# Kernel tuning notes

Measured on AMD Instinct MI355X. Metric: run time of the kernel, lower is better.

Reference implementation:

```python
import jax, jax.numpy as jnp
import numpy as np

B, C, H, W = 1, 64, 128, 128
HEADS, NWIN, TOPK = 8, 16, 4
EPS = 1e-6


def dwconv(x, w, b, pad):
    # x: NCHW, w: (C,1,k,k) depthwise conv weight
    y = jax.lax.conv_general_dilated(
        x, w, (1, 1), [(pad, pad), (pad, pad)],
        dimension_numbers=('NCHW', 'OIHW', 'NCHW'),
        feature_group_count=x.shape[1])
    return y + b[None, :, None, None]


def layernorm(x, g, b):
    m = x.mean(-1, keepdims=True)
    v = ((x - m) ** 2).mean(-1, keepdims=True)
    return (x - m) * jax.lax.rsqrt(v + EPS) * g + b


def drf_attn(x, qkv_w, qkv_b, wo_w, wo_b, lepe_w, lepe_b):
    # x: (B,H,W,C) NHWC, BiFormer-style top-k routed window attention
    Bb, Hh, Ww, Cc = x.shape
    h, w = Hh // NWIN, Ww // NWIN
    hw, p2 = h * w, NWIN * NWIN
    # window partition -> (B, p2, hw, C)
    xw = x.reshape(Bb, NWIN, h, NWIN, w, Cc).transpose(0, 1, 3, 2, 4, 5).reshape(Bb, p2, hw, Cc)
    qkv = xw @ qkv_w + qkv_b                       # (B,p2,hw,3C), qk_dim == dim
    q, kv = qkv[..., :Cc], qkv[..., Cc:]
    # window-level routing: per-window mean q/k
    q_win = q.mean(2)                              # (B,p2,C)
    k_win = kv[..., :Cc].mean(2)                   # (B,p2,C)
    logits = jnp.einsum('bpc,bqc->bpq', q_win, k_win)
    _, idx = jax.lax.top_k(logits, TOPK)           # (B,p2,TOPK) int32
    # gather top-k kv windows for each query window -> (B,p2,TOPK,hw,2C)
    kv_sel = jax.vmap(lambda kvb, ib: kvb[ib])(kv, idx)
    hd = Cc // HEADS
    k_sel = kv_sel[..., :Cc].reshape(Bb, p2, TOPK * hw, HEADS, hd).transpose(0, 1, 3, 2, 4)
    v_sel = kv_sel[..., Cc:].reshape(Bb, p2, TOPK * hw, HEADS, hd).transpose(0, 1, 3, 2, 4)
    q_h = q.reshape(Bb, p2, hw, HEADS, hd).transpose(0, 1, 3, 2, 4)
    scale = Cc ** -0.5                             # qk_dim ** -0.5 as in torch module
    attn = jax.nn.softmax(jnp.einsum('bpnqd,bpnkd->bpnqk', q_h * scale, k_sel), axis=-1)
    out = jnp.einsum('bpnqk,bpnkd->bpnqd', attn, v_sel)
    out = out.transpose(0, 1, 3, 2, 4).reshape(Bb, p2, hw, Cc)
    # un-window -> (B,H,W,C)
    out = out.reshape(Bb, NWIN, NWIN, h, w, Cc).transpose(0, 1, 3, 2, 4, 5).reshape(Bb, Hh, Ww, Cc)
    # LePE: depthwise 5x5 conv on full-image v
    v_full = kv[..., Cc:].reshape(Bb, NWIN, NWIN, h, w, Cc).transpose(0, 1, 3, 2, 4, 5).reshape(Bb, Hh, Ww, Cc)
    lepe = dwconv(v_full.transpose(0, 3, 1, 2), lepe_w, lepe_b, 2).transpose(0, 2, 3, 1)
    return (out + lepe) @ wo_w + wo_b


def setup_inputs() -> dict:
    key = jax.random.key(0)
    ks = jax.random.split(key, 8)
    s = lambda k, shape: jax.random.normal(k, shape, jnp.float32) * 0.02
    return {
        'x': jax.random.normal(ks[0], (B, C, H, W), jnp.float32),
        'pos_w': s(ks[1], (C, 1, 3, 3)), 'pos_b': jnp.zeros((C,), jnp.float32),
        'norm_g': jnp.ones((C,), jnp.float32), 'norm_b': jnp.zeros((C,), jnp.float32),
        'qkv_w': s(ks[2], (C, 3 * C)), 'qkv_b': jnp.zeros((3 * C,), jnp.float32),
        'wo_w': s(ks[3], (C, C)), 'wo_b': jnp.zeros((C,), jnp.float32),
        'lepe_w': s(ks[4], (C, 1, 5, 5)), 'lepe_b': jnp.zeros((C,), jnp.float32),
        'mlp_w1': s(ks[5], (C, 4 * C)), 'mlp_b1': jnp.zeros((4 * C,), jnp.float32),
        'mlp_w2': s(ks[6], (4 * C, C)), 'mlp_b2': jnp.zeros((C,), jnp.float32),
    }


def reference(x, pos_w, pos_b, norm_g, norm_b, qkv_w, qkv_b, wo_w, wo_b,
              lepe_w, lepe_b, mlp_w1, mlp_b1, mlp_w2, mlp_b2):
    x = x + dwconv(x, pos_w, pos_b, 1)             # dwconv pos-embed (NCHW)
    x = x.transpose(0, 2, 3, 1)                    # -> NHWC
    x = x + drf_attn(layernorm(x, norm_g, norm_b), qkv_w, qkv_b, wo_w, wo_b, lepe_w, lepe_b)
    y = layernorm(x, norm_g, norm_b)               # same LayerNorm weights reused
    y = jax.nn.gelu(y @ mlp_w1 + mlp_b1, approximate=False) @ mlp_w2 + mlp_b2
    x = x + y
    return x.transpose(0, 3, 1, 2)                 # -> NCHW
```

## Files before the change

kernel.cpp:

```cpp
#include <hip/hip_runtime.h>
#include <hip/hip_bf16.h>
#include <math.h>

#define HPIX 128
#define WPIX 128
#define NPIX (HPIX*WPIX)
#define CCH 64
#define P2 256
#define HWIN 64
#define LNS 36
#define LNS2 68

__device__ __forceinline__ float waveReduceSum(float v){
  #pragma unroll
  for (int m = 32; m >= 1; m >>= 1) v += __shfl_xor(v, m);
  return v;
}

__device__ __forceinline__ float gelu_exact(float h){
  return 0.5f*h*(1.f + erff(h*0.70710678118654752f));
}

__global__ void k1_posconv(const float* __restrict__ x, const float* __restrict__ pw,
                           const float* __restrict__ pb, float* __restrict__ x1){
  __shared__ float tile[4][3][72];
  __shared__ float lds[4][64];
  int tid = threadIdx.x;
  int pl = tid & 63, cl = tid >> 6;
  int pix0 = (blockIdx.x & 255) * 64;
  int cg   = (blockIdx.x >> 8);
  int c = cg*4 + cl;
  int y  = pix0 >> 7;
  int xb = pix0 & 127;
  const float* xc = x + c*NPIX;
  for (int t = pl; t < 3*66; t += 64){
    int r = t / 66, ccol = t - r*66;
    int yy = y - 1 + r, xxr = xb - 1 + ccol;
    float v = 0.f;
    if ((unsigned)yy < (unsigned)HPIX && (unsigned)xxr < (unsigned)WPIX)
      v = xc[yy*WPIX + xxr];
    tile[cl][r][ccol] = v;
  }
  float wreg[9];
  #pragma unroll
  for (int t=0;t<9;t++) wreg[t] = pw[c*9+t];
  float bias = pb[c];
  __syncthreads();
  float acc = bias;
  #pragma unroll
  for (int dy=0;dy<3;dy++)
    #pragma unroll
    for (int dx=0;dx<3;dx++)
      acc += wreg[dy*3+dx] * tile[cl][dy][pl+dx];
  lds[cl][pl] = tile[cl][1][pl+1] + acc;
  __syncthreads();
  int pp = tid >> 2, cc = tid & 3;
  x1[(pix0+pp)*CCH + cg*4 + cc] = lds[cc][pp];
}

__global__ void k2_ln_qkv(const float* __restrict__ x1,
                          const float* __restrict__ g, const float* __restrict__ bb,
                          const float* __restrict__ qw, const float* __restrict__ qb,
                          float* __restrict__ qkv){
  __shared__ __align__(16) float lnT[64][LNS2];
  int tid = threadIdx.x, w = tid >> 6, lane = tid & 63;
  int pix0 = blockIdx.x * 64;
  #pragma unroll
  for (int i=0; i<8; i++){
    int pl = w*8 + i, pix = pix0 + pl;
    float v = x1[pix*CCH + lane];
    float mean = waveReduceSum(v) * (1.f/64.f);
    float d = v - mean;
    float var = waveReduceSum(d*d) * (1.f/64.f);
    lnT[lane][pl] = d * rsqrtf(var + 1e-6f) * g[lane] + bb[lane];
  }
  __syncthreads();
  int p0 = (tid & 15) * 4;
  int cg = tid >> 4;
  int j0 = cg * 6;
  float acc[4][6];
  #pragma unroll
  for (int i=0;i<4;i++)
    #pragma unroll
    for (int j=0;j<6;j++) acc[i][j] = qb[j0+j];
  for (int k0=0; k0<64; k0+=2){
    float4 a0 = *(const float4*)&lnT[k0][p0];
    float4 a1 = *(const float4*)&lnT[k0+1][p0];
    const float* wr0 = qw + k0*192 + j0;
    const float* wr1 = wr0 + 192;
    float2 u00 = *(const float2*)(wr0);
    float2 u01 = *(const float2*)(wr0+2);
    float2 u02 = *(const float2*)(wr0+4);
    float2 u10 = *(const float2*)(wr1);
    float2 u11 = *(const float2*)(wr1+2);
    float2 u12 = *(const float2*)(wr1+4);
    float a0v[4] = {a0.x,a0.y,a0.z,a0.w};
    float a1v[4] = {a1.x,a1.y,a1.z,a1.w};
    #pragma unroll
    for (int i=0;i<4;i++){
      acc[i][0]+=a0v[i]*u00.x; acc[i][1]+=a0v[i]*u00.y;
      acc[i][2]+=a0v[i]*u01.x; acc[i][3]+=a0v[i]*u01.y;
      acc[i][4]+=a0v[i]*u02.x; acc[i][5]+=a0v[i]*u02.y;
    }
    #pragma unroll
    for (int i=0;i<4;i++){
      acc[i][0]+=a1v[i]*u10.x; acc[i][1]+=a1v[i]*u10.y;
      acc[i][2]+=a1v[i]*u11.x; acc[i][3]+=a1v[i]*u11.y;
      acc[i][4]+=a1v[i]*u12.x; acc[i][5]+=a1v[i]*u12.y;
    }
  }
  int y = pix0 >> 7;
  int pb_row = (y>>3)*16, rrow = (y&7)<<3, xbase = pix0 & 127;
  #pragma unroll
  for (int i=0;i<4;i++){
    int xx = xbase + p0 + i;
    int p = pb_row + (xx>>3);
    int r = rrow + (xx&7);
    float* o = qkv + (p*HWIN + r)*192 + j0;
    *(float2*)(o)     = make_float2(acc[i][0], acc[i][1]);
    *(float2*)(o + 2) = make_float2(acc[i][2], acc[i][3]);
    *(float2*)(o + 4) = make_float2(acc[i][4], acc[i][5]);
  }
}

__global__ void k3_winmean(const float* __restrict__ qkv,
                           float* __restrict__ qwin, float* __restrict__ kwinT){
  int p = blockIdx.x;
  int tid = threadIdx.x, rq = tid >> 6, c = tid & 63;
  float sq = 0.f, sk = 0.f;
  for (int r = rq*16; r < rq*16+16; r++){
    const float* row = qkv + (p*HWIN + r)*192;
    sq += row[c];
    sk += row[64 + c];
  }
  __shared__ float s1[4][64], s2[4][64];
  s1[rq][c] = sq; s2[rq][c] = sk;
  __syncthreads();
  if (tid < 64){
    qwin[p*64 + c]   = (s1[0][c]+s1[1][c]+s1[2][c]+s1[3][c])*(1.f/64.f);
    kwinT[c*P2 + p]  = (s2[0][c]+s2[1][c]+s2[2][c]+s2[3][c])*(1.f/64.f);
  }
}

__global__ void k4_topk(const float* __restrict__ qwin, const float* __restrict__ kwinT,
                        int* __restrict__ idx){
  int p = blockIdx.x, t = threadIdx.x;
  int w = t >> 6, lane = t & 63;
  __shared__ float qs[64];
  __shared__ float lg[P2];
  __shared__ float wv[4]; __shared__ int wi[4];
  if (t < 64) qs[t] = qwin[p*64 + t];
  __syncthreads();
  float acc = 0.f;
  #pragma unroll 8
  for (int c=0; c<64; c++) acc += qs[c] * kwinT[c*P2 + t];
  lg[t] = acc;
  __syncthreads();
  for (int j=0; j<4; j++){
    float v = lg[t]; int i = t;
    #pragma unroll
    for (int m=32; m>=1; m>>=1){
      float ov = __shfl_xor(v, m); int oi = __shfl_xor(i, m);
      if (ov > v || (ov == v && oi < i)){ v = ov; i = oi; }
    }
    if (lane == 0){ wv[w] = v; wi[w] = i; }
    __syncthreads();
    if (t == 0){
      float bv = wv[0]; int bi = wi[0];
      #pragma unroll
      for (int u=1; u<4; u++)
        if (wv[u] > bv || (wv[u] == bv && wi[u] < bi)){ bv = wv[u]; bi = wi[u]; }
      idx[p*4 + j] = bi;
      lg[bi] = -1e30f;
    }
    __syncthreads();
  }
}

__global__ void k5_attn(const float* __restrict__ qkv, const int* __restrict__ idx,
                        float* __restrict__ attnout){
  int p = blockIdx.x >> 3, n = blockIdx.x & 7;
  int tid = threadIdx.x, w = tid >> 6, lane = tid & 63;
  __shared__ float Ks[256][8];
  __shared__ float Vs[256][8];
  __shared__ int wsel[4];
  float* psbuf = &Ks[0][0];
  __shared__ float ps_tail[256];
  (void)ps_tail;
  if (tid < 4) wsel[tid] = idx[p*4 + tid];
  __syncthreads();
  int cb = n*8;
  for (int u = tid; u < 512; u += 256){
    int k = u >> 1, h = u & 1;
    const float* row = qkv + (wsel[k>>6]*HWIN + (k&63))*192;
    *(float4*)&Ks[k][h*4] = *(const float4*)(row + 64  + cb + h*4);
    *(float4*)&Vs[k][h*4] = *(const float4*)(row + 128 + cb + h*4);
  }
  __syncthreads();
  const float* qrow = qkv + (p*HWIN + lane)*192 + cb;
  float4 q0 = *(const float4*)(qrow);
  float4 q1 = *(const float4*)(qrow + 4);
  float q[8] = {q0.x*0.125f, q0.y*0.125f, q0.z*0.125f, q0.w*0.125f,
                q1.x*0.125f, q1.y*0.125f, q1.z*0.125f, q1.w*0.125f};
  float l = 0.f, acc[8];
  #pragma unroll
  for (int d=0; d<8; d++) acc[d] = 0.f;
  #pragma unroll 4
  for (int k = w*64; k < w*64+64; k++){
    float4 ka = *(float4*)&Ks[k][0];
    float4 kb = *(float4*)&Ks[k][4];
    float s = q[0]*ka.x + q[1]*ka.y + q[2]*ka.z + q[3]*ka.w
            + q[4]*kb.x + q[5]*kb.y + q[6]*kb.z + q[7]*kb.w;
    float e = __expf(s);
    l += e;
    float4 va = *(float4*)&Vs[k][0];
    float4 vb = *(float4*)&Vs[k][4];
    acc[0]+=e*va.x; acc[1]+=e*va.y; acc[2]+=e*va.z; acc[3]+=e*va.w;
    acc[4]+=e*vb.x; acc[5]+=e*vb.y; acc[6]+=e*vb.z; acc[7]+=e*vb.w;
  }
  __syncthreads();
  float* myp = psbuf + (w*64 + lane)*9;
  #pragma unroll
  for (int d=0; d<8; d++) myp[d] = acc[d];
  myp[8] = l;
  __syncthreads();
  {
    int qi = (w << 4) + (lane & 15);
    int d0 = (lane >> 4) * 2;
    float L = 0.f, o0 = 0.f, o1 = 0.f;
    #pragma unroll
    for (int u=0; u<4; u++){
      const float* pp2 = psbuf + (u*64 + qi)*9;
      L  += pp2[8];
      o0 += pp2[d0];
      o1 += pp2[d0+1];
    }
    float inv = 1.f / L;
    int yy = (p>>4)*8 + (qi>>3), xx = (p&15)*8 + (qi&7);
    float* orow = attnout + (yy*WPIX + xx)*CCH + cb + d0;
    *(float2*)orow = make_float2(o0*inv, o1*inv);
  }
}

__global__ void k6_lepe_wo(const float* __restrict__ attnout, const float* __restrict__ qkv,
                           const float* __restrict__ lw, const float* __restrict__ lb,
                           const float* __restrict__ ww, const float* __restrict__ wb,
                           float* __restrict__ x1){
  __shared__ float tT[64][LNS];
  int tid = threadIdx.x, w = tid >> 6, lane = tid & 63;
  int pix0 = blockIdx.x * 32;
  for (int i=0; i<8; i++){
    int pl = w*8 + i, pix = pix0 + pl;
    int y = pix >> 7, xx = pix & 127;
    float acc = lb[lane];
    #pragma unroll
    for (int dy=0; dy<5; dy++){
      int yy = y+dy-2; if ((unsigned)yy >= (unsigned)HPIX) continue;
      #pragma unroll
      for (int dx=0; dx<5; dx++){
        int x2 = xx+dx-2; if ((unsigned)x2 >= (unsigned)WPIX) continue;
        int pp = (yy>>3)*16 + (x2>>3), rr = ((yy&7)<<3) + (x2&7);
        acc += lw[lane*25 + dy*5 + dx] * qkv[(pp*HWIN + rr)*192 + 128 + lane];
      }
    }
    tT[lane][pl] = attnout[pix*CCH + lane] + acc;
  }
  __syncthreads();
  int p0 = (tid & 7) * 4;
  int cg = tid >> 3;
  int j0 = cg * 2;
  float a0[4], a1[4];
  #pragma unroll
  for (int i=0;i<4;i++){ a0[i] = wb[j0]; a1[i] = wb[j0+1]; }
  #pragma unroll 4
  for (int k=0; k<64; k++){
    float4 a = *(const float4*)&tT[k][p0];
    float2 u = *(const float2*)(ww + k*64 + j0);
    a0[0]+=a.x*u.x; a1[0]+=a.x*u.y;
    a0[1]+=a.y*u.x; a1[1]+=a.y*u.y;
    a0[2]+=a.z*u.x; a1[2]+=a.z*u.y;
    a0[3]+=a.w*u.x; a1[3]+=a.w*u.y;
  }
  #pragma unroll
  for (int i=0;i<4;i++){
    int pix = pix0 + p0 + i;
    float* xb = x1 + pix*CCH + j0;
    float2 r = *(float2*)xb;
    r.x += a0[i]; r.y += a1[i];
    *(float2*)xb = r;
  }
}

__global__ void k7_mlp_out(const float* __restrict__ x2,
                           const float* __restrict__ g, const float* __restrict__ bb,
                           const float* __restrict__ w1, const float* __restrict__ b1,
                           const float* __restrict__ w2, const float* __restrict__ b2,
                           float* __restrict__ out){
  __shared__ __align__(16) float smem[11520];
  float (*lnT)[LNS]  = (float(*)[LNS])smem;
  float (*hidT)[LNS] = (float(*)[LNS])(smem + 64*LNS);
  float* red = smem;
  int tid = threadIdx.x, w = tid >> 6, lane = tid & 63;
  int pix0 = blockIdx.x * 32;
  #pragma unroll
  for (int i=0; i<8; i++){
    int pl = w*8 + i, pix = pix0 + pl;
    float v = x2[pix*CCH + lane];
    float mean = waveReduceSum(v) * (1.f/64.f);
    float d = v - mean;
    float var = waveReduceSum(d*d) * (1.f/64.f);
    lnT[lane][pl] = d * rsqrtf(var + 1e-6f) * g[lane] + bb[lane];
  }
  __syncthreads();
  {
    int p0 = (tid & 7) * 4;
    int j0 = (tid >> 3) * 8;
    float acc[4][8];
    #pragma unroll
    for (int i=0;i<4;i++)
      #pragma unroll
      for (int j=0;j<8;j++) acc[i][j] = b1[j0+j];
    for (int k0=0; k0<64; k0+=2){
      float4 a0 = *(const float4*)&lnT[k0][p0];
      float4 a1 = *(const float4*)&lnT[k0+1][p0];
      const float* wr0 = w1 + k0*256 + j0;
      const float* wr1 = wr0 + 256;
      float4 u00 = *(const float4*)(wr0);
      float4 u01 = *(const float4*)(wr0+4);
      float4 u10 = *(const float4*)(wr1);
      float4 u11 = *(const float4*)(wr1+4);
      float a0v[4] = {a0.x,a0.y,a0.z,a0.w};
      float a1v[4] = {a1.x,a1.y,a1.z,a1.w};
      #pragma unroll
      for (int i=0;i<4;i++){
        acc[i][0]+=a0v[i]*u00.x; acc[i][1]+=a0v[i]*u00.y;
        acc[i][2]+=a0v[i]*u00.z; acc[i][3]+=a0v[i]*u00.w;
        acc[i][4]+=a0v[i]*u01.x; acc[i][5]+=a0v[i]*u01.y;
        acc[i][6]+=a0v[i]*u01.z; acc[i][7]+=a0v[i]*u01.w;
      }
      #pragma unroll
      for (int i=0;i<4;i++){
        acc[i][0]+=a1v[i]*u10.x; acc[i][1]+=a1v[i]*u10.y;
        acc[i][2]+=a1v[i]*u10.z; acc[i][3]+=a1v[i]*u10.w;
        acc[i][4]+=a1v[i]*u11.x; acc[i][5]+=a1v[i]*u11.y;
        acc[i][6]+=a1v[i]*u11.z; acc[i][7]+=a1v[i]*u11.w;
      }
    }
    #pragma unroll
    for (int j=0;j<8;j++){
      float4 hv;
      hv.x = gelu_exact(acc[0][j]);
      hv.y = gelu_exact(acc[1][j]);
      hv.z = gelu_exact(acc[2][j]);
      hv.w = gelu_exact(acc[3][j]);
      *(float4*)&hidT[j0+j][p0] = hv;
    }
  }
  __syncthreads();
  float acc2[4][8];
  {
    int p0 = (lane & 7) * 4;
    int c0 = (lane >> 3) * 8;
    #pragma unroll
    for (int i=0;i<4;i++)
      #pragma unroll
      for (int j=0;j<8;j++) acc2[i][j] = 0.f;
    int kbase = w*64;
    for (int k0=0; k0<64; k0+=2){
      int k = kbase + k0;
      float4 a0 = *(const float4*)&hidT[k][p0];
      float4 a1 = *(const float4*)&hidT[k+1][p0];
      const float* wr0 = w2 + k*64 + c0;
      const float* wr1 = wr0 + 64;
      float4 u00 = *(const float4*)(wr0);
      float4 u01 = *(const float4*)(wr0+4);
      float4 u10 = *(const float4*)(wr1);
      float4 u11 = *(const float4*)(wr1+4);
      float a0v[4] = {a0.x,a0.y,a0.z,a0.w};
      float a1v[4] = {a1.x,a1.y,a1.z,a1.w};
      #pragma unroll
      for (int i=0;i<4;i++){
        acc2[i][0]+=a0v[i]*u00.x; acc2[i][1]+=a0v[i]*u00.y;
        acc2[i][2]+=a0v[i]*u00.z; acc2[i][3]+=a0v[i]*u00.w;
        acc2[i][4]+=a0v[i]*u01.x; acc2[i][5]+=a0v[i]*u01.y;
        acc2[i][6]+=a0v[i]*u01.z; acc2[i][7]+=a0v[i]*u01.w;
      }
      #pragma unroll
      for (int i=0;i<4;i++){
        acc2[i][0]+=a1v[i]*u10.x; acc2[i][1]+=a1v[i]*u10.y;
        acc2[i][2]+=a1v[i]*u10.z; acc2[i][3]+=a1v[i]*u10.w;
        acc2[i][4]+=a1v[i]*u11.x; acc2[i][5]+=a1v[i]*u11.y;
        acc2[i][6]+=a1v[i]*u11.z; acc2[i][7]+=a1v[i]*u11.w;
      }
    }
  }
  __syncthreads();
  #pragma unroll
  for (int t=0; t<16; t++){
    int s = 2*t, i = s >> 3, j = s & 7;
    *(float2*)&red[tid*34 + s] = make_float2(acc2[i][j], acc2[i][j+1]);
  }
  __syncthreads();
  {
    int lane_r = tid & 63, ir = tid >> 6;
    int pg = lane_r & 7, cgf = lane_r >> 3;
    int pix = pix0 + pg*4 + ir;
    int c0 = cgf*8;
    float o[8];
    #pragma unroll
    for (int j=0;j<8;j++) o[j] = b2[c0+j];
    #pragma unroll
    for (int wq=0; wq<4; wq++){
      const float* rp = &red[(wq*64 + lane_r)*34 + ir*8];
      #pragma unroll
      for (int j2=0;j2<4;j2++){
        float2 pr = *(const float2*)(rp + 2*j2);
        o[2*j2]   += pr.x;
        o[2*j2+1] += pr.y;
      }
    }
    const float* xr = x2 + pix*CCH + c0;
    float4 r0 = *(const float4*)(xr);
    float4 r1 = *(const float4*)(xr+4);
    o[0]+=r0.x; o[1]+=r0.y; o[2]+=r0.z; o[3]+=r0.w;
    o[4]+=r1.x; o[5]+=r1.y; o[6]+=r1.z; o[7]+=r1.w;
    #pragma unroll
    for (int j=0;j<8;j++)
      out[(c0+j)*NPIX + pix] = o[j];
  }
}

extern "C" void kernel_launch(void* const* d_in, const int* in_sizes, int n_in,
                              void* d_out, int out_size, void* d_ws, size_t ws_size,
                              hipStream_t stream) {
  (void)in_sizes; (void)n_in; (void)out_size; (void)ws_size;
  const float* x      = (const float*)d_in[0];
  const float* pos_w  = (const float*)d_in[1];
  const float* pos_b  = (const float*)d_in[2];
  const float* norm_g = (const float*)d_in[3];
  const float* norm_b = (const float*)d_in[4];
  const float* qkv_w  = (const float*)d_in[5];
  const float* qkv_b  = (const float*)d_in[6];
  const float* wo_w   = (const float*)d_in[7];
  const float* wo_b   = (const float*)d_in[8];
  const float* lepe_w = (const float*)d_in[9];
  const float* lepe_b = (const float*)d_in[10];
  const float* mlp_w1 = (const float*)d_in[11];
  const float* mlp_b1 = (const float*)d_in[12];
  const float* mlp_w2 = (const float*)d_in[13];
  const float* mlp_b2 = (const float*)d_in[14];
  float* out = (float*)d_out;

  char* ws = (char*)d_ws;
  float* x1      = (float*)(ws);
  float* qkv     = (float*)(ws + (4u<<20));
  float* qwin    = (float*)(ws + (16u<<20));
  float* kwinT   = (float*)(ws + (16u<<20) + (64u<<10));
  int*   idx     = (int*)  (ws + (16u<<20) + (128u<<10));
  float* attnout = (float*)(ws + (17u<<20));

  hipLaunchKernelGGL(k1_posconv, dim3(4096), dim3(256), 0, stream, x, pos_w, pos_b, x1);
  hipLaunchKernelGGL(k2_ln_qkv,  dim3(256),  dim3(512), 0, stream, x1, norm_g, norm_b, qkv_w, qkv_b, qkv);
  hipLaunchKernelGGL(k3_winmean, dim3(256),  dim3(256), 0, stream, qkv, qwin, kwinT);
  hipLaunchKernelGGL(k4_topk,    dim3(256),  dim3(256), 0, stream, qwin, kwinT, idx);
  hipLaunchKernelGGL(k5_attn,    dim3(2048), dim3(256), 0, stream, qkv, idx, attnout);
  hipLaunchKernelGGL(k6_lepe_wo, dim3(512),  dim3(256), 0, stream, attnout, qkv, lepe_w, lepe_b, wo_w, wo_b, x1);
  hipLaunchKernelGGL(k7_mlp_out, dim3(512),  dim3(256), 0, stream, x1, norm_g, norm_b, mlp_w1, mlp_b1, mlp_w2, mlp_b2, out);
}
```

Baseline: 201.2 us.

## Fuse LePE/Wo projection with MLP kernel and shrink LN-QKV block tile

Merges the LePE+output-projection kernel with the LayerNorm+MLP kernel so the post-attention residual stays in shared memory instead of being written to global x1 and read back. The fused kernel also reuses that shared copy for the final residual add. Separately, the LN+QKV kernel now handles 32 pixels per 256-thread block instead of 64 per 512-thread block, giving more, smaller blocks. The fusion adds a kernel with larger LDS use, which may lower occupancy, and removes one launch.

```diff
diff --git a/kernel.cpp b/kernel.cpp
--- a/kernel.cpp
+++ b/kernel.cpp
@@ -9,7 +9,6 @@
 #define P2 256
 #define HWIN 64
 #define LNS 36
-#define LNS2 68
 
 __device__ __forceinline__ float waveReduceSum(float v){
   #pragma unroll
@@ -62,9 +61,9 @@
                           const float* __restrict__ g, const float* __restrict__ bb,
                           const float* __restrict__ qw, const float* __restrict__ qb,
                           float* __restrict__ qkv){
-  __shared__ __align__(16) float lnT[64][LNS2];
+  __shared__ __align__(16) float lnT[64][LNS];
   int tid = threadIdx.x, w = tid >> 6, lane = tid & 63;
-  int pix0 = blockIdx.x * 64;
+  int pix0 = blockIdx.x * 32;
   #pragma unroll
   for (int i=0; i<8; i++){
     int pl = w*8 + i, pix = pix0 + pl;
@@ -75,8 +74,8 @@
     lnT[lane][pl] = d * rsqrtf(var + 1e-6f) * g[lane] + bb[lane];
   }
   __syncthreads();
-  int p0 = (tid & 15) * 4;
-  int cg = tid >> 4;
+  int p0 = (tid & 7) * 4;
+  int cg = tid >> 3;
   int j0 = cg * 6;
   float acc[4][6];
   #pragma unroll
@@ -184,9 +183,9 @@
   __shared__ float Ks[256][8];
   __shared__ float Vs[256][8];
   __shared__ int wsel[4];
-  float* psbuf = &Ks[0][0];
   __shared__ float ps_tail[256];
   (void)ps_tail;
+  float* psbuf = &Ks[0][0];
   if (tid < 4) wsel[tid] = idx[p*4 + tid];
   __syncthreads();
   int cb = n*8;
@@ -242,13 +241,24 @@
   }
 }
 
-__global__ void k6_lepe_wo(const float* __restrict__ attnout, const float* __restrict__ qkv,
-                           const float* __restrict__ lw, const float* __restrict__ lb,
-                           const float* __restrict__ ww, const float* __restrict__ wb,
-                           float* __restrict__ x1){
-  __shared__ float tT[64][LNS];
+__global__ void k67_lepe_wo_mlp(const float* __restrict__ attnout,
+                                const float* __restrict__ qkv,
+                                const float* __restrict__ lw, const float* __restrict__ lb,
+                                const float* __restrict__ ww, const float* __restrict__ wb,
+                                const float* __restrict__ x1,
+                                const float* __restrict__ g, const float* __restrict__ bb,
+                                const float* __restrict__ w1, const float* __restrict__ b1,
+                                const float* __restrict__ w2, const float* __restrict__ b2,
+                                float* __restrict__ out){
+  __shared__ __align__(16) float smem[13824];
+  float* x2T  = smem;
+  float* lnT  = smem + 2304;
+  float* hidT = smem + 4608;
+  float* tT   = hidT;
+  float* red  = hidT;
   int tid = threadIdx.x, w = tid >> 6, lane = tid & 63;
   int pix0 = blockIdx.x * 32;
+
   for (int i=0; i<8; i++){
     int pl = w*8 + i, pix = pix0 + pl;
     int y = pix >> 7, xx = pix & 127;
@@ -258,60 +268,52 @@
       int yy = y+dy-2; if ((unsigned)yy >= (unsigned)HPIX) continue;
       #pragma unroll
       for (int dx=0; dx<5; dx++){
-        int x2 = xx+dx-2; if ((unsigned)x2 >= (unsigned)WPIX) continue;
-        int pp = (yy>>3)*16 + (x2>>3), rr = ((yy&7)<<3) + (x2&7);
+        int x2c = xx+dx-2; if ((unsigned)x2c >= (unsigned)WPIX) continue;
+        int pp = (yy>>3)*16 + (x2c>>3), rr = ((yy&7)<<3) + (x2c&7);
         acc += lw[lane*25 + dy*5 + dx] * qkv[(pp*HWIN + rr)*192 + 128 + lane];
       }
     }
-    tT[lane][pl] = attnout[pix*CCH + lane] + acc;
-  }
-  __syncthreads();
-  int p0 = (tid & 7) * 4;
-  int cg = tid >> 3;
-  int j0 = cg * 2;
-  float a0[4], a1[4];
-  #pragma unroll
-  for (int i=0;i<4;i++){ a0[i] = wb[j0]; a1[i] = wb[j0+1]; }
-  #pragma unroll 4
-  for (int k=0; k<64; k++){
-    float4 a = *(const float4*)&tT[k][p0];
-    float2 u = *(const float2*)(ww + k*64 + j0);
-    a0[0]+=a.x*u.x; a1[0]+=a.x*u.y;
-    a0[1]+=a.y*u.x; a1[1]+=a.y*u.y;
-    a0[2]+=a.z*u.x; a1[2]+=a.z*u.y;
-    a0[3]+=a.w*u.x; a1[3]+=a.w*u.y;
-  }
-  #pragma unroll
-  for (int i=0;i<4;i++){
-    int pix = pix0 + p0 + i;
-    float* xb = x1 + pix*CCH + j0;
-    float2 r = *(float2*)xb;
-    r.x += a0[i]; r.y += a1[i];
-    *(float2*)xb = r;
-  }
-}
-
-__global__ void k7_mlp_out(const float* __restrict__ x2,
-                           const float* __restrict__ g, const float* __restrict__ bb,
-                           const float* __restrict__ w1, const float* __restrict__ b1,
-                           const float* __restrict__ w2, const float* __restrict__ b2,
-                           float* __restrict__ out){
-  __shared__ __align__(16) float smem[11520];
-  float (*lnT)[LNS]  = (float(*)[LNS])smem;
-  float (*hidT)[LNS] = (float(*)[LNS])(smem + 64*LNS);
-  float* red = smem;
-  int tid = threadIdx.x, w = tid >> 6, lane = tid & 63;
-  int pix0 = blockIdx.x * 32;
+    tT[lane*LNS + pl] = attnout[pix*CCH + lane] + acc;
+  }
+  __syncthreads();
+
+  {
+    int p0 = (tid & 7) * 4;
+    int cg = tid >> 3;
+    int j0 = cg * 2;
+    float a0[4], a1[4];
+    #pragma unroll
+    for (int i=0;i<4;i++){ a0[i] = wb[j0]; a1[i] = wb[j0+1]; }
+    #pragma unroll 4
+    for (int k=0; k<64; k++){
+      float4 a = *(const float4*)&tT[k*LNS + p0];
+      float2 u = *(const float2*)(ww + k*64 + j0);
+      a0[0]+=a.x*u.x; a1[0]+=a.x*u.y;
+      a0[1]+=a.y*u.x; a1[1]+=a.y*u.y;
+      a0[2]+=a.z*u.x; a1[2]+=a.z*u.y;
+      a0[3]+=a.w*u.x; a1[3]+=a.w*u.y;
+    }
+    #pragma unroll
+    for (int i=0;i<4;i++){
+      int pix = pix0 + p0 + i;
+      float2 r = *(const float2*)(x1 + pix*CCH + j0);
+      x2T[j0*LNS + p0 + i]     = r.x + a0[i];
+      x2T[(j0+1)*LNS + p0 + i] = r.y + a1[i];
+    }
+  }
+  __syncthreads();
+
   #pragma unroll
   for (int i=0; i<8; i++){
-    int pl = w*8 + i, pix = pix0 + pl;
-    float v = x2[pix*CCH + lane];
+    int pl = w*8 + i;
+    float v = x2T[lane*LNS + pl];
     float mean = waveReduceSum(v) * (1.f/64.f);
     float d = v - mean;
     float var = waveReduceSum(d*d) * (1.f/64.f);
-    lnT[lane][pl] = d * rsqrtf(var + 1e-6f) * g[lane] + bb[lane];
-  }
-  __syncthreads();
+    lnT[lane*LNS + pl] = d * rsqrtf(var + 1e-6f) * g[lane] + bb[lane];
+  }
+  __syncthreads();
+
   {
     int p0 = (tid & 7) * 4;
     int j0 = (tid >> 3) * 8;
@@ -321,8 +323,8 @@
       #pragma unroll
       for (int j=0;j<8;j++) acc[i][j] = b1[j0+j];
     for (int k0=0; k0<64; k0+=2){
-      float4 a0 = *(const float4*)&lnT[k0][p0];
-      float4 a1 = *(const float4*)&lnT[k0+1][p0];
+      float4 a0 = *(const float4*)&lnT[k0*LNS + p0];
+      float4 a1 = *(const float4*)&lnT[(k0+1)*LNS + p0];
       const float* wr0 = w1 + k0*256 + j0;
       const float* wr1 = wr0 + 256;
       float4 u00 = *(const float4*)(wr0);
@@ -353,10 +355,11 @@
       hv.y = gelu_exact(acc[1][j]);
       hv.z = gelu_exact(acc[2][j]);
       hv.w = gelu_exact(acc[3][j]);
-      *(float4*)&hidT[j0+j][p0] = hv;
-    }
-  }
-  __syncthreads();
+      *(float4*)&hidT[(j0+j)*LNS + p0] = hv;
+    }
+  }
+  __syncthreads();
+
   float acc2[4][8];
   {
     int p0 = (lane & 7) * 4;
@@ -368,8 +371,8 @@
     int kbase = w*64;
     for (int k0=0; k0<64; k0+=2){
       int k = kbase + k0;
-      float4 a0 = *(const float4*)&hidT[k][p0];
-      float4 a1 = *(const float4*)&hidT[k+1][p0];
+      float4 a0 = *(const float4*)&hidT[k*LNS + p0];
+      float4 a1 = *(const float4*)&hidT[(k+1)*LNS + p0];
       const float* wr0 = w2 + k*64 + c0;
       const float* wr1 = wr0 + 64;
       float4 u00 = *(const float4*)(wr0);
@@ -401,6 +404,7 @@
     *(float2*)&red[tid*34 + s] = make_float2(acc2[i][j], acc2[i][j+1]);
   }
   __syncthreads();
+
   {
     int lane_r = tid & 63, ir = tid >> 6;
     int pg = lane_r & 7, cgf = lane_r >> 3;
@@ -419,11 +423,10 @@
         o[2*j2+1] += pr.y;
       }
     }
-    const float* xr = x2 + pix*CCH + c0;
-    float4 r0 = *(const float4*)(xr);
-    float4 r1 = *(const float4*)(xr+4);
-    o[0]+=r0.x; o[1]+=r0.y; o[2]+=r0.z; o[3]+=r0.w;
-    o[4]+=r1.x; o[5]+=r1.y; o[6]+=r1.z; o[7]+=r1.w;
+    int plocal = pg*4 + ir;
+    #pragma unroll
+    for (int j=0;j<8;j++)
+      o[j] += x2T[(c0+j)*LNS + plocal];
     #pragma unroll
     for (int j=0;j<8;j++)
       out[(c0+j)*NPIX + pix] = o[j];
@@ -459,11 +462,12 @@
   int*   idx     = (int*)  (ws + (16u<<20) + (128u<<10));
   float* attnout = (float*)(ws + (17u<<20));
 
-  hipLaunchKernelGGL(k1_posconv, dim3(4096), dim3(256), 0, stream, x, pos_w, pos_b, x1);
-  hipLaunchKernelGGL(k2_ln_qkv,  dim3(256),  dim3(512), 0, stream, x1, norm_g, norm_b, qkv_w, qkv_b, qkv);
-  hipLaunchKernelGGL(k3_winmean, dim3(256),  dim3(256), 0, stream, qkv, qwin, kwinT);
-  hipLaunchKernelGGL(k4_topk,    dim3(256),  dim3(256), 0, stream, qwin, kwinT, idx);
-  hipLaunchKernelGGL(k5_attn,    dim3(2048), dim3(256), 0, stream, qkv, idx, attnout);
-  hipLaunchKernelGGL(k6_lepe_wo, dim3(512),  dim3(256), 0, stream, attnout, qkv, lepe_w, lepe_b, wo_w, wo_b, x1);
-  hipLaunchKernelGGL(k7_mlp_out, dim3(512),  dim3(256), 0, stream, x1, norm_g, norm_b, mlp_w1, mlp_b1, mlp_w2, mlp_b2, out);
-}
+  hipLaunchKernelGGL(k1_posconv,      dim3(4096), dim3(256), 0, stream, x, pos_w, pos_b, x1);
+  hipLaunchKernelGGL(k2_ln_qkv,       dim3(512),  dim3(256), 0, stream, x1, norm_g, norm_b, qkv_w, qkv_b, qkv);
+  hipLaunchKernelGGL(k3_winmean,      dim3(256),  dim3(256), 0, stream, qkv, qwin, kwinT);
+  hipLaunchKernelGGL(k4_topk,         dim3(256),  dim3(256), 0, stream, qwin, kwinT, idx);
+  hipLaunchKernelGGL(k5_attn,         dim3(2048), dim3(256), 0, stream, qkv, idx, attnout);
+  hipLaunchKernelGGL(k67_lepe_wo_mlp, dim3(512),  dim3(256), 0, stream, attnout, qkv,
+                     lepe_w, lepe_b, wo_w, wo_b, x1, norm_g, norm_b,
+                     mlp_w1, mlp_b1, mlp_w2, mlp_b2, out);
+}
```

Result: no change. 197.9 us (-1.6%).
